# Kernel optimization log

Measured on AMD Instinct MI355X. Metric: run time of the kernel, lower is better.

## Reference

```python
import jax, jax.numpy as jnp
import numpy as np

B, L, D = 16, 2048, 320          # batch, frames, stacked feature dim (80 mel * 4 reduction)
CODEBOOK_SIZE, CODEBOOK_DIM = 8192, 16


def setup_inputs() -> dict:
    key = jax.random.key(0)
    k1, k2, k3 = jax.random.split(key, 3)
    masked_target_values = jax.random.normal(k1, (B, L, D), dtype=jnp.float32)
    # xavier_uniform_ for shape (D, codebook_dim): bound = sqrt(6/(fan_in+fan_out))
    bound = np.sqrt(6.0 / (D + CODEBOOK_DIM)).astype(np.float32)
    project_mat = jax.random.uniform(k2, (D, CODEBOOK_DIM), dtype=jnp.float32,
                                     minval=-bound, maxval=bound)
    cb = jax.random.normal(k3, (CODEBOOK_SIZE, CODEBOOK_DIM), dtype=jnp.float32)
    codebook_norm = cb / jnp.maximum(jnp.linalg.norm(cb, axis=-1, keepdims=True), 1e-12)
    return {"masked_target_values": masked_target_values,
            "project_mat": project_mat,
            "codebook_norm": codebook_norm}


def reference(masked_target_values, project_mat, codebook_norm):
    # project: (B, L, D) @ (D, K) -> (B, L, K)
    targets = jnp.einsum('bld,dk->blk', masked_target_values, project_mat)
    # L2 normalize along last dim (torch F.normalize with eps=1e-12)
    targets_norm = targets / jnp.maximum(
        jnp.linalg.norm(targets, axis=-1, keepdims=True), 1e-12)
    x2 = jnp.sum(targets_norm * targets_norm, axis=-1, keepdims=True)      # (B, L, 1)
    c2 = jnp.sum(codebook_norm * codebook_norm, axis=-1)                   # (C,)
    xc = jnp.einsum('blk,ck->blc', targets_norm, codebook_norm)            # (B, L, C)
    d2 = jnp.maximum(x2 + c2[None, None, :] - 2.0 * xc, 0.0)
    vector_distances = jnp.sqrt(d2)
    labels = jnp.argmin(vector_distances, axis=-1)                         # (B, L) int
    return labels
```

## Files before the change

### kernel.cpp

```cpp
#include <hip/hip_runtime.h>
#include <cfloat>

#define TOKENS 32768
#define DIM    320
#define NCODE  8192
#define PROW   20
#define APAD   40
#define NTILE  64
#define CERT_UNITS 32u

typedef __attribute__((ext_vector_type(8)))  short short8;
typedef __attribute__((ext_vector_type(16))) float f32x16;
typedef unsigned short ushort_t;
typedef unsigned int   uint_t;

static __device__ __forceinline__ ushort_t f2bf(float f) {
    uint_t u = __float_as_uint(f);
    u += 0x7fffu + ((u >> 16) & 1u);
    return (ushort_t)(u >> 16);
}
static __device__ __forceinline__ float bf2f(ushort_t h) {
    return __uint_as_float(((uint_t)h) << 16);
}
static __device__ __forceinline__ uint_t pack2(ushort_t a, ushort_t b) {
    return (uint_t)a | ((uint_t)b << 16);
}
static __device__ __forceinline__ uint_t umaxu(uint_t a, uint_t b) { return a > b ? a : b; }
static __device__ __forceinline__ uint_t uminu(uint_t a, uint_t b) { return a < b ? a : b; }

__global__ __launch_bounds__(256) void pack_kernel(
    const float* __restrict__ cb,
    float* __restrict__ c2o,
    ushort_t* __restrict__ cbpack)
{
    int j = blockIdx.x * 256 + threadIdx.x;
    const float4* cr4 = (const float4*)(cb + (size_t)j * 16);
    float4 c0 = cr4[0], c1 = cr4[1], c2v = cr4[2], c3 = cr4[3];
    float c[16] = {c0.x, c0.y, c0.z, c0.w, c1.x, c1.y, c1.z, c1.w,
                   c2v.x, c2v.y, c2v.z, c2v.w, c3.x, c3.y, c3.z, c3.w};
    float s = 0.f;
    #pragma unroll
    for (int k = 0; k < 16; ++k) s = fmaf(c[k], c[k], s);
    c2o[j] = s;
    ushort_t hi[16], lo[16];
    #pragma unroll
    for (int k = 0; k < 16; ++k) {
        hi[k] = f2bf(c[k]);
        lo[k] = f2bf(c[k] - bf2f(hi[k]));
    }
    uint4* dst = (uint4*)(cbpack + (size_t)j * 32);
    dst[0] = make_uint4(pack2(hi[0], hi[1]), pack2(hi[2], hi[3]),
                        pack2(hi[4], hi[5]), pack2(hi[6], hi[7]));
    dst[1] = make_uint4(pack2(hi[8], hi[9]), pack2(hi[10], hi[11]),
                        pack2(hi[12], hi[13]), pack2(hi[14], hi[15]));
    dst[2] = make_uint4(pack2(lo[0], lo[1]), pack2(lo[2], lo[3]),
                        pack2(lo[4], lo[5]), pack2(lo[6], lo[7]));
    dst[3] = make_uint4(pack2(lo[8], lo[9]), pack2(lo[10], lo[11]),
                        pack2(lo[12], lo[13]), pack2(lo[14], lo[15]));
}

__global__ __launch_bounds__(256, 4) void fused_kernel(
    const float* __restrict__ x,
    const float* __restrict__ P,
    const float* __restrict__ cb,
    const float* __restrict__ c2g,
    const ushort_t* __restrict__ cbpack,
    int* __restrict__ out)
{
    __shared__ float Ps[DIM * PROW];
    __shared__ ushort_t ApackS[32 * APAD];
    __shared__ float tnS[32 * 16];
    __shared__ float x2S[32];
    __shared__ uint_t mergeS[4][32][2];
    __shared__ int flagS[36];
    __shared__ float redE[4];
    __shared__ int   redI[4];

    int tid = threadIdx.x;
    if (tid == 0) flagS[32] = 0;

    {
        const float4* P4 = (const float4*)P;
        #pragma unroll
        for (int i = 0; i < 5; ++i) {
            int idx = tid + i * 256;
            int row = idx >> 2, col = idx & 3;
            *(float4*)(Ps + row * PROW + col * 4) = P4[idx];
        }
    }
    __syncthreads();

    int sub = tid & 7;
    int tk  = tid >> 3;
    int tok = blockIdx.x * 32 + tk;
    {
        const float* xr = x + (size_t)tok * DIM;
        float acc[16];
        #pragma unroll
        for (int k = 0; k < 16; ++k) acc[k] = 0.f;
        for (int i = 0; i < 40; ++i) {
            int d = i * 8 + sub;
            float xv = xr[d];
            const float4* pr = (const float4*)(Ps + d * PROW);
            float4 p0 = pr[0], p1 = pr[1], p2 = pr[2], p3 = pr[3];
            acc[0] = fmaf(xv, p0.x, acc[0]);   acc[1] = fmaf(xv, p0.y, acc[1]);
            acc[2] = fmaf(xv, p0.z, acc[2]);   acc[3] = fmaf(xv, p0.w, acc[3]);
            acc[4] = fmaf(xv, p1.x, acc[4]);   acc[5] = fmaf(xv, p1.y, acc[5]);
            acc[6] = fmaf(xv, p1.z, acc[6]);   acc[7] = fmaf(xv, p1.w, acc[7]);
            acc[8] = fmaf(xv, p2.x, acc[8]);   acc[9] = fmaf(xv, p2.y, acc[9]);
            acc[10] = fmaf(xv, p2.z, acc[10]); acc[11] = fmaf(xv, p2.w, acc[11]);
            acc[12] = fmaf(xv, p3.x, acc[12]); acc[13] = fmaf(xv, p3.y, acc[13]);
            acc[14] = fmaf(xv, p3.z, acc[14]); acc[15] = fmaf(xv, p3.w, acc[15]);
        }
        #pragma unroll
        for (int m = 1; m <= 4; m <<= 1) {
            #pragma unroll
            for (int k = 0; k < 16; ++k)
                acc[k] += __shfl_xor(acc[k], m);
        }
        float ss = 0.f;
        #pragma unroll
        for (int k = 0; k < 16; ++k) ss = fmaf(acc[k], acc[k], ss);
        float nrm = fmaxf(sqrtf(ss), 1e-12f);
        float inv = 1.0f / nrm;
        float t[16];
        #pragma unroll
        for (int k = 0; k < 16; ++k) t[k] = acc[k] * inv;
        float xx = 0.f;
        #pragma unroll
        for (int k = 0; k < 16; ++k) xx = fmaf(t[k], t[k], xx);

        ushort_t hi[16], lo[16];
        #pragma unroll
        for (int k = 0; k < 16; ++k) {
            hi[k] = f2bf(t[k]);
            lo[k] = f2bf(t[k] - bf2f(hi[k]));
        }
        if (sub < 4) {
            *(float4*)(tnS + tk * 16 + sub * 4) =
                make_float4(t[4 * sub], t[4 * sub + 1], t[4 * sub + 2], t[4 * sub + 3]);
        }
        uint4* dst = (uint4*)(ApackS + tk * APAD);
        if (sub == 4) dst[0] = make_uint4(pack2(hi[0], hi[1]), pack2(hi[2], hi[3]),
                                          pack2(hi[4], hi[5]), pack2(hi[6], hi[7]));
        if (sub == 5) dst[1] = make_uint4(pack2(hi[8], hi[9]), pack2(hi[10], hi[11]),
                                          pack2(hi[12], hi[13]), pack2(hi[14], hi[15]));
        if (sub == 6) dst[2] = make_uint4(pack2(lo[0], lo[1]), pack2(lo[2], lo[3]),
                                          pack2(lo[4], lo[5]), pack2(lo[6], lo[7]));
        if (sub == 7) dst[3] = make_uint4(pack2(lo[8], lo[9]), pack2(lo[10], lo[11]),
                                          pack2(lo[12], lo[13]), pack2(lo[14], lo[15]));
        if (sub == 0) x2S[tk] = xx;
    }
    __syncthreads();

    int lane = tid & 63;
    int wave = tid >> 6;
    int half = lane >> 5;
    int l31  = lane & 31;
    {
        short8 hiA = *(const short8*)(ApackS + l31 * APAD + half * 8);
        short8 loA = *(const short8*)(ApackS + l31 * APAD + 16 + half * 8);

        f32x16 zero = {};
        asm volatile("" : "+v"(zero));
        uint_t p1[16], p2[16];
        #pragma unroll
        for (int r = 0; r < 16; ++r) { p1[r] = 0u; p2[r] = 0u; }

        for (int t = 0; t < NTILE; ++t) {
            int crow = wave * (NTILE * 32) + t * 32 + l31;
            const ushort_t* cp = cbpack + (size_t)crow * 32;
            short8 hiB = *(const short8*)(cp + half * 8);
            short8 loB = *(const short8*)(cp + 16 + half * 8);

            f32x16 acc = __builtin_amdgcn_mfma_f32_32x32x16_bf16(hiA, hiB, zero, 0, 0, 0);
            asm volatile("" : "+v"(acc));
            acc = __builtin_amdgcn_mfma_f32_32x32x16_bf16(loA, hiB, acc, 0, 0, 0);
            asm volatile("" : "+v"(acc));
            acc = __builtin_amdgcn_mfma_f32_32x32x16_bf16(hiA, loB, acc, 0, 0, 0);
            asm volatile("" : "+v"(acc));

            uint_t inv = 8191u - (uint_t)crow;
            #pragma unroll
            for (int r = 0; r < 16; ++r) {
                float kf = fmaf(acc[r], 131072.0f, 131072.0f);
                uint_t ku = (uint_t)kf;
                uint_t p  = (ku << 13) | inv;
                p2[r] = umaxu(p2[r], uminu(p, p1[r]));
                p1[r] = umaxu(p1[r], p);
            }
        }
        #pragma unroll
        for (int mask = 1; mask <= 16; mask <<= 1) {
            #pragma unroll
            for (int r = 0; r < 16; ++r) {
                uint_t a1 = (uint_t)__shfl_xor((int)p1[r], mask);
                uint_t a2 = (uint_t)__shfl_xor((int)p2[r], mask);
                uint_t np2 = umaxu(uminu(p1[r], a1), umaxu(p2[r], a2));
                p1[r] = umaxu(p1[r], a1);
                p2[r] = np2;
            }
        }
        #pragma unroll
        for (int r = 0; r < 16; ++r) {
            if (l31 == r) {
                int mrow = (r & 3) + 8 * (r >> 2) + 4 * half;
                mergeS[wave][mrow][0] = p1[r];
                mergeS[wave][mrow][1] = p2[r];
            }
        }
    }
    __syncthreads();

    if (tid < 32) {
        uint_t p1 = mergeS[0][tid][0], p2 = mergeS[0][tid][1];
        #pragma unroll
        for (int w = 1; w < 4; ++w) {
            uint_t a1 = mergeS[w][tid][0];
            uint_t a2 = mergeS[w][tid][1];
            uint_t np2 = umaxu(uminu(p1, a1), umaxu(p2, a2));
            p1 = umaxu(p1, a1);
            p2 = np2;
        }
        if ((p1 >> 13) - (p2 >> 13) <= CERT_UNITS) {
            int pz = atomicAdd(&flagS[32], 1);
            flagS[pz] = tid;
        } else {
            out[blockIdx.x * 32 + tid] = 8191 - (int)(p1 & 8191u);
        }
    }
    __syncthreads();

    int nf = flagS[32];
    for (int fi = 0; fi < nf; ++fi) {
        int ftk = flagS[fi];
        float a[16];
        #pragma unroll
        for (int k = 0; k < 16; ++k) a[k] = tnS[ftk * 16 + k];
        float xx = x2S[ftk];
        float mn = FLT_MAX;
        int   id = 0x7fffffff;
        for (int c = 0; c < 32; ++c) {
            int j = c * 256 + tid;
            const float4* c4 = (const float4*)(cb + (size_t)j * 16);
            float4 c0 = c4[0], c1 = c4[1], c2v = c4[2], c3 = c4[3];
            float dot = 0.f;
            dot = fmaf(a[0], c0.x, dot);   dot = fmaf(a[1], c0.y, dot);
            dot = fmaf(a[2], c0.z, dot);   dot = fmaf(a[3], c0.w, dot);
            dot = fmaf(a[4], c1.x, dot);   dot = fmaf(a[5], c1.y, dot);
            dot = fmaf(a[6], c1.z, dot);   dot = fmaf(a[7], c1.w, dot);
            dot = fmaf(a[8], c2v.x, dot);  dot = fmaf(a[9], c2v.y, dot);
            dot = fmaf(a[10], c2v.z, dot); dot = fmaf(a[11], c2v.w, dot);
            dot = fmaf(a[12], c3.x, dot);  dot = fmaf(a[13], c3.y, dot);
            dot = fmaf(a[14], c3.z, dot);  dot = fmaf(a[15], c3.w, dot);
            float e = fmaf(-2.f, dot, xx + c2g[j]);
            if (e < mn || (e == mn && j < id)) { mn = e; id = j; }
        }
        #pragma unroll
        for (int mask = 1; mask <= 32; mask <<= 1) {
            float pmn = __shfl_xor(mn, mask);
            int   pid = __shfl_xor(id, mask);
            if (pmn < mn || (pmn == mn && pid < id)) { mn = pmn; id = pid; }
        }
        if (lane == 0) { redE[wave] = mn; redI[wave] = id; }
        __syncthreads();
        if (tid == 0) {
            #pragma unroll
            for (int w = 1; w < 4; ++w) {
                float pe = redE[w]; int pi = redI[w];
                if (pe < mn || (pe == mn && pi < id)) { mn = pe; id = pi; }
            }
            out[blockIdx.x * 32 + ftk] = id;
        }
        __syncthreads();
    }
}

extern "C" void kernel_launch(void* const* d_in, const int* in_sizes, int n_in,
                              void* d_out, int out_size, void* d_ws, size_t ws_size,
                              hipStream_t stream) {
    const float* x   = (const float*)d_in[0];
    const float* P   = (const float*)d_in[1];
    const float* cbn = (const float*)d_in[2];

    float*    c2     = (float*)d_ws;
    ushort_t* cbpack = (ushort_t*)(c2 + NCODE);
    int* labels = (int*)d_out;

    pack_kernel<<<NCODE / 256, 256, 0, stream>>>(cbn, c2, cbpack);
    fused_kernel<<<TOKENS / 32, 256, 0, stream>>>(x, P, cbn, c2, cbpack, labels);
}
```

Baseline: 175.4 us.

## Software-pipeline codebook MFMA tiles in pairs and use float-bit argmax keys

The codebook scan is restructured to process two 32-code tiles per iteration. The next pair's loads and MFMAs are issued after the current pair's top-2 key reduction, so matrix work overlaps the integer max/min updates. Keys are now built by masking the float bits of (dot+1.0625) instead of an fma plus float-to-int conversion, and the certification test is redone in float space with a fixed epsilon. Launch bounds drop from 4 to 2 waves per SIMD to leave room for the extra accumulators, which trades occupancy for ILP.

Measured after the change: 225.6 us. 28.6% more time.

```diff
diff --git a/kernel.cpp b/kernel.cpp
--- a/kernel.cpp
+++ b/kernel.cpp
@@ -7,7 +7,7 @@
 #define PROW   20
 #define APAD   40
 #define NTILE  64
-#define CERT_UNITS 32u
+#define EPS_CERT 3e-4f
 
 typedef __attribute__((ext_vector_type(8)))  short short8;
 typedef __attribute__((ext_vector_type(16))) float f32x16;
@@ -27,6 +27,9 @@
 }
 static __device__ __forceinline__ uint_t umaxu(uint_t a, uint_t b) { return a > b ? a : b; }
 static __device__ __forceinline__ uint_t uminu(uint_t a, uint_t b) { return a < b ? a : b; }
+static __device__ __forceinline__ uint_t mkkey(float v, uint_t inv) {
+    return (__float_as_uint(v + 1.0625f) & 0xFFFFE000u) | inv;
+}
 
 __global__ __launch_bounds__(256) void pack_kernel(
     const float* __restrict__ cb,
@@ -59,7 +62,7 @@
                         pack2(lo[12], lo[13]), pack2(lo[14], lo[15]));
 }
 
-__global__ __launch_bounds__(256, 4) void fused_kernel(
+__global__ __launch_bounds__(256, 2) void fused_kernel(
     const float* __restrict__ x,
     const float* __restrict__ P,
     const float* __restrict__ cb,
@@ -162,34 +165,66 @@
         short8 loA = *(const short8*)(ApackS + l31 * APAD + 16 + half * 8);
 
         f32x16 zero = {};
-        asm volatile("" : "+v"(zero));
         uint_t p1[16], p2[16];
         #pragma unroll
         for (int r = 0; r < 16; ++r) { p1[r] = 0u; p2[r] = 0u; }
 
-        for (int t = 0; t < NTILE; ++t) {
-            int crow = wave * (NTILE * 32) + t * 32 + l31;
-            const ushort_t* cp = cbpack + (size_t)crow * 32;
-            short8 hiB = *(const short8*)(cp + half * 8);
-            short8 loB = *(const short8*)(cp + 16 + half * 8);
-
-            f32x16 acc = __builtin_amdgcn_mfma_f32_32x32x16_bf16(hiA, hiB, zero, 0, 0, 0);
-            asm volatile("" : "+v"(acc));
-            acc = __builtin_amdgcn_mfma_f32_32x32x16_bf16(loA, hiB, acc, 0, 0, 0);
-            asm volatile("" : "+v"(acc));
-            acc = __builtin_amdgcn_mfma_f32_32x32x16_bf16(hiA, loB, acc, 0, 0, 0);
-            asm volatile("" : "+v"(acc));
-
-            uint_t inv = 8191u - (uint_t)crow;
+        int base = wave * (NTILE * 32) + l31;
+
+        const ushort_t* cpa = cbpack + (size_t)base * 32;
+        const ushort_t* cpb = cbpack + (size_t)(base + 32) * 32;
+        short8 hiBa = *(const short8*)(cpa + half * 8);
+        short8 loBa = *(const short8*)(cpa + 16 + half * 8);
+        short8 hiBb = *(const short8*)(cpb + half * 8);
+        short8 loBb = *(const short8*)(cpb + 16 + half * 8);
+        f32x16 acc0 = __builtin_amdgcn_mfma_f32_32x32x16_bf16(hiA, hiBa, zero, 0, 0, 0);
+        acc0 = __builtin_amdgcn_mfma_f32_32x32x16_bf16(loA, hiBa, acc0, 0, 0, 0);
+        acc0 = __builtin_amdgcn_mfma_f32_32x32x16_bf16(hiA, loBa, acc0, 0, 0, 0);
+        f32x16 acc1 = __builtin_amdgcn_mfma_f32_32x32x16_bf16(hiA, hiBb, zero, 0, 0, 0);
+        acc1 = __builtin_amdgcn_mfma_f32_32x32x16_bf16(loA, hiBb, acc1, 0, 0, 0);
+        acc1 = __builtin_amdgcn_mfma_f32_32x32x16_bf16(hiA, loBb, acc1, 0, 0, 0);
+        uint_t inv0 = 8191u - (uint_t)base;
+        uint_t inv1 = 8191u - (uint_t)(base + 32);
+
+        #pragma unroll 1
+        for (int pt = 1; pt < NTILE / 2; ++pt) {
+            int crow = base + pt * 64;
+            const ushort_t* cpa2 = cbpack + (size_t)crow * 32;
+            const ushort_t* cpb2 = cbpack + (size_t)(crow + 32) * 32;
+            short8 nhiBa = *(const short8*)(cpa2 + half * 8);
+            short8 nloBa = *(const short8*)(cpa2 + 16 + half * 8);
+            short8 nhiBb = *(const short8*)(cpb2 + half * 8);
+            short8 nloBb = *(const short8*)(cpb2 + 16 + half * 8);
+
             #pragma unroll
             for (int r = 0; r < 16; ++r) {
-                float kf = fmaf(acc[r], 131072.0f, 131072.0f);
-                uint_t ku = (uint_t)kf;
-                uint_t p  = (ku << 13) | inv;
-                p2[r] = umaxu(p2[r], uminu(p, p1[r]));
-                p1[r] = umaxu(p1[r], p);
+                uint_t a = mkkey(acc0[r], inv0);
+                uint_t b = mkkey(acc1[r], inv1);
+                uint_t pm = umaxu(a, b);
+                uint_t pn = uminu(a, b);
+                p2[r] = umaxu(umaxu(p2[r], uminu(p1[r], pm)), pn);
+                p1[r] = umaxu(p1[r], pm);
             }
-        }
+
+            acc0 = __builtin_amdgcn_mfma_f32_32x32x16_bf16(hiA, nhiBa, zero, 0, 0, 0);
+            acc0 = __builtin_amdgcn_mfma_f32_32x32x16_bf16(loA, nhiBa, acc0, 0, 0, 0);
+            acc0 = __builtin_amdgcn_mfma_f32_32x32x16_bf16(hiA, nloBa, acc0, 0, 0, 0);
+            acc1 = __builtin_amdgcn_mfma_f32_32x32x16_bf16(hiA, nhiBb, zero, 0, 0, 0);
+            acc1 = __builtin_amdgcn_mfma_f32_32x32x16_bf16(loA, nhiBb, acc1, 0, 0, 0);
+            acc1 = __builtin_amdgcn_mfma_f32_32x32x16_bf16(hiA, nloBb, acc1, 0, 0, 0);
+            inv0 = 8191u - (uint_t)crow;
+            inv1 = 8191u - (uint_t)(crow + 32);
+        }
+        #pragma unroll
+        for (int r = 0; r < 16; ++r) {
+            uint_t a = mkkey(acc0[r], inv0);
+            uint_t b = mkkey(acc1[r], inv1);
+            uint_t pm = umaxu(a, b);
+            uint_t pn = uminu(a, b);
+            p2[r] = umaxu(umaxu(p2[r], uminu(p1[r], pm)), pn);
+            p1[r] = umaxu(p1[r], pm);
+        }
+
         #pragma unroll
         for (int mask = 1; mask <= 16; mask <<= 1) {
             #pragma unroll
@@ -222,7 +257,9 @@
             p1 = umaxu(p1, a1);
             p2 = np2;
         }
-        if ((p1 >> 13) - (p2 >> 13) <= CERT_UNITS) {
+        float f1lo = __uint_as_float(p1 & 0xFFFFE000u);
+        float f2hi = __uint_as_float((p2 & 0xFFFFE000u) + 0x2000u);
+        if (f1lo - f2hi <= EPS_CERT) {
             int pz = atomicAdd(&flagS[32], 1);
             flagS[pz] = tid;
         } else {
```
